# Optimization experiments

Measured on AMD Instinct MI355X. Metric: run time of the kernel, lower is better.

The kernel has to match this reference:

```python
import jax, jax.numpy as jnp
import numpy as np

EMBED_DIM = 1024
HEAD_DIM = 64
B, S = 16, 2048


def setup_inputs() -> dict:
    key = jax.random.key(0)
    ks = jax.random.split(key, 8)
    scale = 1.0 / np.sqrt(EMBED_DIM)
    return {
        "x": jax.random.normal(ks[0], (B, S, EMBED_DIM), dtype=jnp.float32),
        "mask": jax.random.randint(ks[1], (B, S), 0, 2, dtype=jnp.int32),
        "Wq": jax.random.normal(ks[2], (EMBED_DIM, HEAD_DIM), dtype=jnp.float32) * scale,
        "bq": jnp.zeros((HEAD_DIM,), dtype=jnp.float32),
        "Wk": jax.random.normal(ks[3], (EMBED_DIM, HEAD_DIM), dtype=jnp.float32) * scale,
        "bk": jnp.zeros((HEAD_DIM,), dtype=jnp.float32),
        "Wv": jax.random.normal(ks[4], (EMBED_DIM, HEAD_DIM), dtype=jnp.float32) * scale,
        "bv": jnp.zeros((HEAD_DIM,), dtype=jnp.float32),
    }


def reference(x, mask, Wq, bq, Wk, bk, Wv, bv):
    # x: [B,S,E], mask: [B,S] with 0 = masked, 1 = keep
    q = x @ Wq + bq          # [B,S,D]
    k = x @ Wk + bk          # [B,S,D]
    v = x @ Wv + bv          # [B,S,D]
    scores = jnp.einsum("bsd,btd->bst", q, k) / jnp.sqrt(jnp.float32(HEAD_DIM))
    scores = jnp.where(mask[:, None, :] == 0, jnp.float32(-1e9), scores)
    attn = jax.nn.softmax(scores, axis=-1)  # [B,S,S]
    return jnp.einsum("bst,btd->bsd", attn, v)  # [B,S,D]
```

## Files before the change

kernel.cpp:

```cpp
#include <hip/hip_runtime.h>
#include <math.h>

#define EMBED 1024
#define HDIM  64
#define BATCH 16
#define SEQ   2048
#define MTOT  (BATCH*SEQ)
#define NE    (MTOT*HDIM)

typedef _Float16 f16;
typedef __attribute__((ext_vector_type(8))) _Float16 half8;
typedef __attribute__((ext_vector_type(4))) _Float16 half4;
typedef __attribute__((ext_vector_type(4))) float  float4v;

__global__ void wprep_kernel(const float* __restrict__ Wq, const float* __restrict__ Wk,
                             const float* __restrict__ Wv, f16* __restrict__ Wt)
{
    int e = blockIdx.x * 256 + threadIdx.x;
    if (e >= 192 * EMBED) return;
    int gn = e >> 10, k = e & 1023;
    int mat = gn >> 6, n = gn & 63;
    const float* W = (mat == 0) ? Wq : ((mat == 1) ? Wk : Wv);
    Wt[e] = (f16)W[k * HDIM + n];
}

__global__ __launch_bounds__(256)
void qkv_mfma_kernel(const float* __restrict__ X, const f16* __restrict__ Wt,
                     const float* __restrict__ bq, const float* __restrict__ bk, const float* __restrict__ bv,
                     f16* __restrict__ Q, f16* __restrict__ K, f16* __restrict__ Vt)
{
    __shared__ f16 Xs[64 * 72];
    __shared__ f16 Csv[64 * 72];

    const int tid  = threadIdx.x;
    const int wave = tid >> 6;
    const int lane = tid & 63;
    const int quad = lane >> 4;
    const int c16  = lane & 15;
    const int m0   = blockIdx.x * 64;
    const int gnb  = wave * 3;

    float4v acc[4][3];
    #pragma unroll
    for (int mt = 0; mt < 4; ++mt)
        #pragma unroll
        for (int nt = 0; nt < 3; ++nt)
            acc[mt][nt] = (float4v){0.f, 0.f, 0.f, 0.f};

    float4 pf[4];
    #pragma unroll
    for (int i = 0; i < 4; ++i) {
        int c = tid + 256 * i, m = c >> 4, ko = (c & 15) * 4;
        pf[i] = *(const float4*)(X + (size_t)(m0 + m) * EMBED + ko);
    }

    for (int k0 = 0; k0 < EMBED; k0 += 64) {
        half8 bh[2][3];
        #pragma unroll
        for (int ks = 0; ks < 2; ++ks)
            #pragma unroll
            for (int nt = 0; nt < 3; ++nt)
                bh[ks][nt] = *(const half8*)(Wt + (size_t)((gnb + nt) * 16 + c16) * EMBED
                                             + k0 + ks * 32 + quad * 8);

        __syncthreads();
        #pragma unroll
        for (int i = 0; i < 4; ++i) {
            int c = tid + 256 * i, m = c >> 4, ko = (c & 15) * 4;
            half4 h = { (f16)pf[i].x, (f16)pf[i].y, (f16)pf[i].z, (f16)pf[i].w };
            *(half4*)&Xs[m * 72 + ko] = h;
        }
        __syncthreads();

        {
            int k1 = (k0 + 64) & (EMBED - 1);
            #pragma unroll
            for (int i = 0; i < 4; ++i) {
                int c = tid + 256 * i, m = c >> 4, ko = (c & 15) * 4;
                pf[i] = *(const float4*)(X + (size_t)(m0 + m) * EMBED + k1 + ko);
            }
        }

        #pragma unroll
        for (int ks = 0; ks < 2; ++ks) {
            half8 a[4];
            #pragma unroll
            for (int mt = 0; mt < 4; ++mt)
                a[mt] = *(const half8*)&Xs[(mt * 16 + c16) * 72 + ks * 32 + quad * 8];
            #pragma unroll
            for (int mt = 0; mt < 4; ++mt)
                #pragma unroll
                for (int nt = 0; nt < 3; ++nt)
                    acc[mt][nt] = __builtin_amdgcn_mfma_f32_16x16x32_f16(a[mt], bh[ks][nt], acc[mt][nt], 0, 0, 0);
        }
    }

    float bb[3];
    #pragma unroll
    for (int nt = 0; nt < 3; ++nt) {
        int gn = (gnb + nt) * 16 + c16, mat = gn >> 6, cn = gn & 63;
        bb[nt] = ((mat == 0) ? bq : ((mat == 1) ? bk : bv))[cn];
    }

    #pragma unroll
    for (int mt = 0; mt < 4; ++mt)
        #pragma unroll
        for (int nt = 0; nt < 3; ++nt) {
            int gn = (gnb + nt) * 16 + c16, mat = gn >> 6, cn = gn & 63;
            if (mat < 2) {
                f16* O = mat ? K : Q;
                #pragma unroll
                for (int r = 0; r < 4; ++r)
                    O[(size_t)(m0 + mt * 16 + quad * 4 + r) * HDIM + cn] =
                        (f16)(acc[mt][nt][r] + bb[nt]);
            }
        }

    __syncthreads();
    #pragma unroll
    for (int mt = 0; mt < 4; ++mt)
        #pragma unroll
        for (int nt = 0; nt < 3; ++nt) {
            int gn = (gnb + nt) * 16 + c16, mat = gn >> 6, cn = gn & 63;
            if (mat == 2) {
                #pragma unroll
                for (int r = 0; r < 4; ++r)
                    Csv[cn * 72 + mt * 16 + quad * 4 + r] = (f16)(acc[mt][nt][r] + bb[nt]);
            }
        }
    __syncthreads();
    {
        int d = tid >> 2, ms = (tid & 3) * 16;
        #pragma unroll
        for (int j = 0; j < 2; ++j)
            *(half8*)(Vt + (size_t)d * MTOT + m0 + ms + 8 * j) =
                *(const half8*)&Csv[d * 72 + ms + 8 * j];
    }
}

__global__ __launch_bounds__(128)
void attn_mfma_kernel(const f16* __restrict__ Q, const f16* __restrict__ K,
                      const f16* __restrict__ Vt, const int* __restrict__ mask,
                      float* __restrict__ out)
{
    __shared__ f16 Ks[2][64 * 72];
    __shared__ f16 Vs[2][64 * 72];
    __shared__ f16 Ps[2][32 * 72];

    const int tid  = threadIdx.x;
    const int wave = tid >> 6;
    const int lane = tid & 63;
    const int quad = lane >> 4;
    const int c16  = lane & 15;
    const int b    = blockIdx.y;
    const int s0   = blockIdx.x * 64;
    const int q0   = s0 + wave * 32;

    half8 qa[2][2];
    #pragma unroll
    for (int qt = 0; qt < 2; ++qt) {
        const size_t qrow = (size_t)(b * SEQ + q0 + qt * 16 + c16) * HDIM;
        qa[qt][0] = *(const half8*)(Q + qrow + quad * 8);
        qa[qt][1] = *(const half8*)(Q + qrow + 32 + quad * 8);
    }

    const half8 ones = { (f16)1.f, (f16)1.f, (f16)1.f, (f16)1.f,
                         (f16)1.f, (f16)1.f, (f16)1.f, (f16)1.f };

    float4v O[2][4];
    #pragma unroll
    for (int qt = 0; qt < 2; ++qt)
        #pragma unroll
        for (int dt = 0; dt < 4; ++dt) O[qt][dt] = (float4v){0.f, 0.f, 0.f, 0.f};
    float4v lacc[2];
    lacc[0] = (float4v){0.f, 0.f, 0.f, 0.f};
    lacc[1] = (float4v){0.f, 0.f, 0.f, 0.f};

    const size_t kbase = (size_t)b * SEQ * HDIM;
    const int vcol0 = b * SEQ;

    half8 pfK[4], pfV[4];
    #pragma unroll
    for (int i = 0; i < 4; ++i) {
        int c = tid + 128 * i, j = c >> 3, o = (c & 7) * 8;
        pfK[i] = *(const half8*)(K  + kbase + (size_t)j * HDIM + o);
        pfV[i] = *(const half8*)(Vt + (size_t)j * MTOT + vcol0 + o);
    }
    int mnext = mask[b * SEQ + lane];

    int cur = 0;
    for (int t0 = 0; t0 < SEQ; t0 += 64) {
        #pragma unroll
        for (int i = 0; i < 4; ++i) {
            int c = tid + 128 * i, j = c >> 3, o = (c & 7) * 8;
            *(half8*)&Ks[cur][j * 72 + o] = pfK[i];
            *(half8*)&Vs[cur][j * 72 + o] = pfV[i];
        }
        int mcur = mnext;

        {
            int t1 = (t0 + 64) & (SEQ - 1);
            #pragma unroll
            for (int i = 0; i < 4; ++i) {
                int c = tid + 128 * i, j = c >> 3, o = (c & 7) * 8;
                pfK[i] = *(const half8*)(K  + kbase + (size_t)(t1 + j) * HDIM + o);
                pfV[i] = *(const half8*)(Vt + (size_t)j * MTOT + vcol0 + t1 + o);
            }
            mnext = mask[b * SEQ + t1 + lane];
        }

        __syncthreads();

        int mk[4];
        #pragma unroll
        for (int nt = 0; nt < 4; ++nt) mk[nt] = __shfl(mcur, nt * 16 + c16, 64);

        float4v s[2][4];
        #pragma unroll
        for (int nt = 0; nt < 4; ++nt) {
            const int krow = (nt * 16 + c16) * 72;
            half8 kh0 = *(const half8*)&Ks[cur][krow + quad * 8];
            half8 kh1 = *(const half8*)&Ks[cur][krow + 32 + quad * 8];
            #pragma unroll
            for (int qt = 0; qt < 2; ++qt) {
                float4v a = (float4v){0.f, 0.f, 0.f, 0.f};
                a = __builtin_amdgcn_mfma_f32_16x16x32_f16(qa[qt][0], kh0, a, 0, 0, 0);
                a = __builtin_amdgcn_mfma_f32_16x16x32_f16(qa[qt][1], kh1, a, 0, 0, 0);
                s[qt][nt] = a;
            }
        }

        #pragma unroll
        for (int qt = 0; qt < 2; ++qt)
            #pragma unroll
            for (int nt = 0; nt < 4; ++nt) {
                #pragma unroll
                for (int r = 0; r < 4; ++r) {
                    float t = fmaf(s[qt][nt][r], 0.125f, -6.0f);
                    t = mk[nt] ? t : -1e30f;
                    Ps[wave][(qt * 16 + quad * 4 + r) * 72 + nt * 16 + c16] = (f16)__expf(t);
                }
            }

        half8 pa[2][2];
        #pragma unroll
        for (int qt = 0; qt < 2; ++qt) {
            const int prow = (qt * 16 + c16) * 72;
            pa[qt][0] = *(const half8*)&Ps[wave][prow + quad * 8];
            pa[qt][1] = *(const half8*)&Ps[wave][prow + 32 + quad * 8];
        }
        #pragma unroll
        for (int qt = 0; qt < 2; ++qt) {
            lacc[qt] = __builtin_amdgcn_mfma_f32_16x16x32_f16(pa[qt][0], ones, lacc[qt], 0, 0, 0);
            lacc[qt] = __builtin_amdgcn_mfma_f32_16x16x32_f16(pa[qt][1], ones, lacc[qt], 0, 0, 0);
        }
        #pragma unroll
        for (int dt = 0; dt < 4; ++dt) {
            const int vrow = (dt * 16 + c16) * 72;
            half8 vh0 = *(const half8*)&Vs[cur][vrow + quad * 8];
            half8 vh1 = *(const half8*)&Vs[cur][vrow + 32 + quad * 8];
            #pragma unroll
            for (int qt = 0; qt < 2; ++qt) {
                O[qt][dt] = __builtin_amdgcn_mfma_f32_16x16x32_f16(pa[qt][0], vh0, O[qt][dt], 0, 0, 0);
                O[qt][dt] = __builtin_amdgcn_mfma_f32_16x16x32_f16(pa[qt][1], vh1, O[qt][dt], 0, 0, 0);
            }
        }

        cur ^= 1;
    }

    #pragma unroll
    for (int qt = 0; qt < 2; ++qt)
        #pragma unroll
        for (int r = 0; r < 4; ++r) {
            float inv = 1.0f / lacc[qt][r];
            size_t orow = (size_t)(b * SEQ + q0 + qt * 16 + quad * 4 + r) * HDIM;
            #pragma unroll
            for (int dt = 0; dt < 4; ++dt)
                out[orow + dt * 16 + c16] = O[qt][dt][r] * inv;
        }
}

extern "C" void kernel_launch(void* const* d_in, const int* in_sizes, int n_in,
                              void* d_out, int out_size, void* d_ws, size_t ws_size,
                              hipStream_t stream) {
    const float* x    = (const float*)d_in[0];
    const int*   mask = (const int*)  d_in[1];
    const float* Wq   = (const float*)d_in[2];
    const float* bq   = (const float*)d_in[3];
    const float* Wk   = (const float*)d_in[4];
    const float* bk   = (const float*)d_in[5];
    const float* Wv   = (const float*)d_in[6];
    const float* bv   = (const float*)d_in[7];
    float* out = (float*)d_out;

    f16* Qf = (f16*)d_ws;
    f16* Kf = Qf + (size_t)NE;
    f16* Vt = Kf + (size_t)NE;
    f16* Wt = Vt + (size_t)NE;

    wprep_kernel<<<dim3(768), dim3(256), 0, stream>>>(Wq, Wk, Wv, Wt);

    qkv_mfma_kernel<<<dim3(MTOT / 64), dim3(256), 0, stream>>>(
        x, Wt, bq, bk, bv, Qf, Kf, Vt);

    attn_mfma_kernel<<<dim3(SEQ / 64, BATCH), dim3(128), 0, stream>>>(
        Qf, Kf, Vt, mask, out);
}
```

Before: 278.6 us.

## Split attention over key halves with 32x32 MFMA and a combine pass

The attention kernel now splits the key sequence into two halves along a new grid dimension, which doubles the block count. Each half writes unnormalized partial outputs and row sums, and a new combine kernel adds them and normalizes. The inner loop moves from 16x16x32 MFMA to 32x32 MFMA tiles. Scores are computed transposed so the probabilities stay in registers, which removes the LDS round trip for P and the ones-matrix MFMA used for the row sums. The mask is now read through a ballot. In exchange it adds extra global traffic for the fp32 partial outputs and one more kernel launch.

New measurement: 264.9 us. 4.9% less time.

```diff
diff --git a/kernel.cpp b/kernel.cpp
--- a/kernel.cpp
+++ b/kernel.cpp
@@ -12,6 +12,7 @@
 typedef __attribute__((ext_vector_type(8))) _Float16 half8;
 typedef __attribute__((ext_vector_type(4))) _Float16 half4;
 typedef __attribute__((ext_vector_type(4))) float  float4v;
+typedef __attribute__((ext_vector_type(16))) float float16v;
 
 __global__ void wprep_kernel(const float* __restrict__ Wq, const float* __restrict__ Wk,
                              const float* __restrict__ Wv, f16* __restrict__ Wt)
@@ -67,8 +68,8 @@
         #pragma unroll
         for (int i = 0; i < 4; ++i) {
             int c = tid + 256 * i, m = c >> 4, ko = (c & 15) * 4;
-            half4 h = { (f16)pf[i].x, (f16)pf[i].y, (f16)pf[i].z, (f16)pf[i].w };
-            *(half4*)&Xs[m * 72 + ko] = h;
+            *(half4*)&Xs[m * 72 + ko] =
+                (half4){ (f16)pf[i].x, (f16)pf[i].y, (f16)pf[i].z, (f16)pf[i].w };
         }
         __syncthreads();
 
@@ -141,40 +142,33 @@
 __global__ __launch_bounds__(128)
 void attn_mfma_kernel(const f16* __restrict__ Q, const f16* __restrict__ K,
                       const f16* __restrict__ Vt, const int* __restrict__ mask,
-                      float* __restrict__ out)
+                      float* __restrict__ Opart0, float* __restrict__ Opart1,
+                      float* __restrict__ Lpart)
 {
     __shared__ f16 Ks[2][64 * 72];
     __shared__ f16 Vs[2][64 * 72];
-    __shared__ f16 Ps[2][32 * 72];
 
     const int tid  = threadIdx.x;
     const int wave = tid >> 6;
     const int lane = tid & 63;
-    const int quad = lane >> 4;
-    const int c16  = lane & 15;
+    const int r31  = lane & 31;
+    const int h5   = lane >> 5;
     const int b    = blockIdx.y;
+    const int kh   = blockIdx.z;
     const int s0   = blockIdx.x * 64;
     const int q0   = s0 + wave * 32;
-
-    half8 qa[2][2];
-    #pragma unroll
-    for (int qt = 0; qt < 2; ++qt) {
-        const size_t qrow = (size_t)(b * SEQ + q0 + qt * 16 + c16) * HDIM;
-        qa[qt][0] = *(const half8*)(Q + qrow + quad * 8);
-        qa[qt][1] = *(const half8*)(Q + qrow + 32 + quad * 8);
-    }
-
-    const half8 ones = { (f16)1.f, (f16)1.f, (f16)1.f, (f16)1.f,
-                         (f16)1.f, (f16)1.f, (f16)1.f, (f16)1.f };
-
-    float4v O[2][4];
-    #pragma unroll
-    for (int qt = 0; qt < 2; ++qt)
-        #pragma unroll
-        for (int dt = 0; dt < 4; ++dt) O[qt][dt] = (float4v){0.f, 0.f, 0.f, 0.f};
-    float4v lacc[2];
-    lacc[0] = (float4v){0.f, 0.f, 0.f, 0.f};
-    lacc[1] = (float4v){0.f, 0.f, 0.f, 0.f};
+    const int kv0  = kh * (SEQ / 2);
+
+    half8 qb[4];
+    {
+        const size_t qrow = (size_t)(b * SEQ + q0 + r31) * HDIM;
+        #pragma unroll
+        for (int i = 0; i < 4; ++i)
+            qb[i] = *(const half8*)(Q + qrow + i * 16 + h5 * 8);
+    }
+
+    float16v O0 = {0.f}, O1 = {0.f};
+    float la[4] = {0.f, 0.f, 0.f, 0.f};
 
     const size_t kbase = (size_t)b * SEQ * HDIM;
     const int vcol0 = b * SEQ;
@@ -183,102 +177,116 @@
     #pragma unroll
     for (int i = 0; i < 4; ++i) {
         int c = tid + 128 * i, j = c >> 3, o = (c & 7) * 8;
-        pfK[i] = *(const half8*)(K  + kbase + (size_t)j * HDIM + o);
-        pfV[i] = *(const half8*)(Vt + (size_t)j * MTOT + vcol0 + o);
-    }
-    int mnext = mask[b * SEQ + lane];
+        pfK[i] = *(const half8*)(K  + kbase + (size_t)(kv0 + j) * HDIM + o);
+        pfV[i] = *(const half8*)(Vt + (size_t)j * MTOT + vcol0 + kv0 + o);
+    }
+    int mreg = mask[b * SEQ + kv0 + lane];
 
     int cur = 0;
-    for (int t0 = 0; t0 < SEQ; t0 += 64) {
+    for (int t = 0; t < SEQ / 2; t += 64) {
         #pragma unroll
         for (int i = 0; i < 4; ++i) {
             int c = tid + 128 * i, j = c >> 3, o = (c & 7) * 8;
             *(half8*)&Ks[cur][j * 72 + o] = pfK[i];
             *(half8*)&Vs[cur][j * 72 + o] = pfV[i];
         }
-        int mcur = mnext;
+        int mcur = mreg;
 
         {
-            int t1 = (t0 + 64) & (SEQ - 1);
+            int t1 = (t + 64) & (SEQ / 2 - 1);
             #pragma unroll
             for (int i = 0; i < 4; ++i) {
                 int c = tid + 128 * i, j = c >> 3, o = (c & 7) * 8;
-                pfK[i] = *(const half8*)(K  + kbase + (size_t)(t1 + j) * HDIM + o);
-                pfV[i] = *(const half8*)(Vt + (size_t)j * MTOT + vcol0 + t1 + o);
-            }
-            mnext = mask[b * SEQ + t1 + lane];
+                pfK[i] = *(const half8*)(K  + kbase + (size_t)(kv0 + t1 + j) * HDIM + o);
+                pfV[i] = *(const half8*)(Vt + (size_t)j * MTOT + vcol0 + kv0 + t1 + o);
+            }
+            mreg = mask[b * SEQ + kv0 + t1 + lane];
         }
 
         __syncthreads();
 
-        int mk[4];
-        #pragma unroll
-        for (int nt = 0; nt < 4; ++nt) mk[nt] = __shfl(mcur, nt * 16 + c16, 64);
-
-        float4v s[2][4];
-        #pragma unroll
-        for (int nt = 0; nt < 4; ++nt) {
-            const int krow = (nt * 16 + c16) * 72;
-            half8 kh0 = *(const half8*)&Ks[cur][krow + quad * 8];
-            half8 kh1 = *(const half8*)&Ks[cur][krow + 32 + quad * 8];
-            #pragma unroll
-            for (int qt = 0; qt < 2; ++qt) {
-                float4v a = (float4v){0.f, 0.f, 0.f, 0.f};
-                a = __builtin_amdgcn_mfma_f32_16x16x32_f16(qa[qt][0], kh0, a, 0, 0, 0);
-                a = __builtin_amdgcn_mfma_f32_16x16x32_f16(qa[qt][1], kh1, a, 0, 0, 0);
-                s[qt][nt] = a;
-            }
-        }
-
-        #pragma unroll
-        for (int qt = 0; qt < 2; ++qt)
-            #pragma unroll
-            for (int nt = 0; nt < 4; ++nt) {
-                #pragma unroll
-                for (int r = 0; r < 4; ++r) {
-                    float t = fmaf(s[qt][nt][r], 0.125f, -6.0f);
-                    t = mk[nt] ? t : -1e30f;
-                    Ps[wave][(qt * 16 + quad * 4 + r) * 72 + nt * 16 + c16] = (f16)__expf(t);
-                }
-            }
-
-        half8 pa[2][2];
-        #pragma unroll
-        for (int qt = 0; qt < 2; ++qt) {
-            const int prow = (qt * 16 + c16) * 72;
-            pa[qt][0] = *(const half8*)&Ps[wave][prow + quad * 8];
-            pa[qt][1] = *(const half8*)&Ps[wave][prow + 32 + quad * 8];
-        }
-        #pragma unroll
-        for (int qt = 0; qt < 2; ++qt) {
-            lacc[qt] = __builtin_amdgcn_mfma_f32_16x16x32_f16(pa[qt][0], ones, lacc[qt], 0, 0, 0);
-            lacc[qt] = __builtin_amdgcn_mfma_f32_16x16x32_f16(pa[qt][1], ones, lacc[qt], 0, 0, 0);
-        }
-        #pragma unroll
-        for (int dt = 0; dt < 4; ++dt) {
-            const int vrow = (dt * 16 + c16) * 72;
-            half8 vh0 = *(const half8*)&Vs[cur][vrow + quad * 8];
-            half8 vh1 = *(const half8*)&Vs[cur][vrow + 32 + quad * 8];
-            #pragma unroll
-            for (int qt = 0; qt < 2; ++qt) {
-                O[qt][dt] = __builtin_amdgcn_mfma_f32_16x16x32_f16(pa[qt][0], vh0, O[qt][dt], 0, 0, 0);
-                O[qt][dt] = __builtin_amdgcn_mfma_f32_16x16x32_f16(pa[qt][1], vh1, O[qt][dt], 0, 0, 0);
-            }
+        unsigned long long bits = __ballot(mcur != 0);
+        unsigned long long shb  = bits >> (4 * h5);
+        unsigned w0 = (unsigned)shb, w1 = (unsigned)(shb >> 32);
+
+        float16v sa = {0.f}, sb = {0.f};
+        #pragma unroll
+        for (int i = 0; i < 4; ++i) {
+            half8 ka0 = *(const half8*)&Ks[cur][(r31)      * 72 + i * 16 + h5 * 8];
+            half8 ka1 = *(const half8*)&Ks[cur][(32 + r31) * 72 + i * 16 + h5 * 8];
+            sa = __builtin_amdgcn_mfma_f32_32x32x16_f16(ka0, qb[i], sa, 0, 0, 0);
+            sb = __builtin_amdgcn_mfma_f32_32x32x16_f16(ka1, qb[i], sb, 0, 0, 0);
+        }
+
+        half4 pa0[4], pa1[4];
+        #pragma unroll
+        for (int g = 0; g < 4; ++g) {
+            #pragma unroll
+            for (int j2 = 0; j2 < 4; ++j2) {
+                const int r  = 4 * g + j2;
+                const int pc = (r & 3) + 8 * (r >> 2);
+                float t0 = fmaf(sa[r], 0.125f, -6.0f);
+                if (!((w0 >> pc) & 1)) t0 = -1e30f;
+                f16 p0 = (f16)__expf(t0);
+                pa0[g][j2] = p0;
+                float t1 = fmaf(sb[r], 0.125f, -6.0f);
+                if (!((w1 >> pc) & 1)) t1 = -1e30f;
+                f16 p1 = (f16)__expf(t1);
+                pa1[g][j2] = p1;
+                la[j2] += (float)p0 + (float)p1;
+            }
+        }
+
+        #pragma unroll
+        for (int g = 0; g < 4; ++g) {
+            const int c0 = g * 8 + h5 * 4;
+            const int c1 = 32 + c0;
+            half4 vA0 = *(const half4*)&Vs[cur][(r31)      * 72 + c0];
+            half4 vA1 = *(const half4*)&Vs[cur][(r31)      * 72 + c1];
+            half4 vB0 = *(const half4*)&Vs[cur][(32 + r31) * 72 + c0];
+            half4 vB1 = *(const half4*)&Vs[cur][(32 + r31) * 72 + c1];
+            O0 = __builtin_amdgcn_mfma_f32_32x32x8f16(pa0[g], vA0, O0, 0, 0, 0);
+            O0 = __builtin_amdgcn_mfma_f32_32x32x8f16(pa1[g], vA1, O0, 0, 0, 0);
+            O1 = __builtin_amdgcn_mfma_f32_32x32x8f16(pa0[g], vB0, O1, 0, 0, 0);
+            O1 = __builtin_amdgcn_mfma_f32_32x32x8f16(pa1[g], vB1, O1, 0, 0, 0);
         }
 
         cur ^= 1;
     }
 
-    #pragma unroll
-    for (int qt = 0; qt < 2; ++qt)
-        #pragma unroll
-        for (int r = 0; r < 4; ++r) {
-            float inv = 1.0f / lacc[qt][r];
-            size_t orow = (size_t)(b * SEQ + q0 + qt * 16 + quad * 4 + r) * HDIM;
-            #pragma unroll
-            for (int dt = 0; dt < 4; ++dt)
-                out[orow + dt * 16 + c16] = O[qt][dt][r] * inv;
-        }
+    float lsum = (la[0] + la[1]) + (la[2] + la[3]);
+    lsum += __shfl_xor(lsum, 32, 64);
+    if (lane < 32)
+        Lpart[(size_t)kh * MTOT + b * SEQ + q0 + lane] = lsum;
+
+    float* Ob = kh ? Opart1 : Opart0;
+    #pragma unroll
+    for (int r = 0; r < 16; ++r) {
+        int q = (r & 3) + 8 * (r >> 2) + 4 * h5;
+        size_t row = (size_t)(b * SEQ + q0 + q) * HDIM;
+        Ob[row + r31]      = O0[r];
+        Ob[row + 32 + r31] = O1[r];
+    }
+}
+
+__global__ __launch_bounds__(256)
+void combine_kernel(const float* __restrict__ Op1, const float* __restrict__ Lp,
+                    float* __restrict__ out)
+{
+    int e = (blockIdx.x * 256 + threadIdx.x) * 8;
+    int m = e >> 6;
+    float inv = 1.0f / (Lp[m] + Lp[MTOT + m]);
+    float4 a0 = *(const float4*)(out + e);
+    float4 a1 = *(const float4*)(out + e + 4);
+    float4 b0 = *(const float4*)(Op1 + e);
+    float4 b1 = *(const float4*)(Op1 + e + 4);
+    float4 r0, r1;
+    r0.x = (a0.x + b0.x) * inv;  r0.y = (a0.y + b0.y) * inv;
+    r0.z = (a0.z + b0.z) * inv;  r0.w = (a0.w + b0.w) * inv;
+    r1.x = (a1.x + b1.x) * inv;  r1.y = (a1.y + b1.y) * inv;
+    r1.z = (a1.z + b1.z) * inv;  r1.w = (a1.w + b1.w) * inv;
+    *(float4*)(out + e)     = r0;
+    *(float4*)(out + e + 4) = r1;
 }
 
 extern "C" void kernel_launch(void* const* d_in, const int* in_sizes, int n_in,
@@ -298,12 +306,17 @@
     f16* Kf = Qf + (size_t)NE;
     f16* Vt = Kf + (size_t)NE;
     f16* Wt = Vt + (size_t)NE;
+    float* Opart1 = (float*)(Wt + 192 * EMBED);
+    float* Lpart  = Opart1 + (size_t)MTOT * HDIM;
 
     wprep_kernel<<<dim3(768), dim3(256), 0, stream>>>(Wq, Wk, Wv, Wt);
 
     qkv_mfma_kernel<<<dim3(MTOT / 64), dim3(256), 0, stream>>>(
         x, Wt, bq, bk, bv, Qf, Kf, Vt);
 
-    attn_mfma_kernel<<<dim3(SEQ / 64, BATCH), dim3(128), 0, stream>>>(
-        Qf, Kf, Vt, mask, out);
-}
+    attn_mfma_kernel<<<dim3(SEQ / 64, BATCH, 2), dim3(128), 0, stream>>>(
+        Qf, Kf, Vt, mask, out, Opart1, Lpart);
+
+    combine_kernel<<<dim3((MTOT * HDIM) / (256 * 8)), dim3(256), 0, stream>>>(
+        Opart1, Lpart, out);
+}
```
